# Performance work log

Measured on AMD Instinct MI355X. Metric: run time of the kernel, lower is better.

The kernel has to match this reference:

```python
import jax, jax.numpy as jnp
import numpy as np

B, P, D = 8, 576, 1024
H = 16
HD = D // H  # 64
HID = 4 * D  # 4096
EPS = 1e-6  # flax LayerNorm default


def _ln(x, g, b):
    m = jnp.mean(x, axis=-1, keepdims=True)
    v = jnp.var(x, axis=-1, keepdims=True)
    return (x - m) * jax.lax.rsqrt(v + EPS) * g + b


def setup_inputs() -> dict:
    key = jax.random.key(0)
    ks = jax.random.split(key, 8)
    s = 0.02
    return {
        "x": jax.random.normal(ks[0], (B, P, D), dtype=jnp.float32),
        "w_qkv": jax.random.normal(ks[1], (D, 3 * D), dtype=jnp.float32) * s,
        "q_g": jnp.ones((HD,), jnp.float32), "q_b": jnp.zeros((HD,), jnp.float32),
        "k_g": jnp.ones((HD,), jnp.float32), "k_b": jnp.zeros((HD,), jnp.float32),
        "o_g": jnp.ones((D,), jnp.float32), "o_b": jnp.zeros((D,), jnp.float32),
        "w_proj": jax.random.normal(ks[2], (D, D), dtype=jnp.float32) * s,
        "b_proj": jnp.zeros((D,), jnp.float32),
        "ln1_g": jnp.ones((D,), jnp.float32), "ln1_b": jnp.zeros((D,), jnp.float32),
        "ln2_g": jnp.ones((D,), jnp.float32), "ln2_b": jnp.zeros((D,), jnp.float32),
        "w1": jax.random.normal(ks[3], (D, HID), dtype=jnp.float32) * s,
        "b1": jnp.zeros((HID,), jnp.float32),
        "w2": jax.random.normal(ks[4], (HID, D), dtype=jnp.float32) * s,
        "b2": jnp.zeros((D,), jnp.float32),
        "ls1": jnp.full((D,), 1e-5, jnp.float32),
        "ls2": jnp.full((D,), 1e-5, jnp.float32),
    }


def reference(x, w_qkv, q_g, q_b, k_g, k_b, o_g, o_b, w_proj, b_proj,
              ln1_g, ln1_b, ln2_g, ln2_b, w1, b1, w2, b2, ls1, ls2):
    scale = HD ** (-0.5)
    # --- attention branch ---
    o = _ln(x, ln1_g, ln1_b)
    qkv = jnp.einsum('bpd,de->bpe', o, w_qkv)
    qkv = qkv.reshape(B, P, 3, H, HD).transpose(2, 0, 3, 1, 4)  # [3,B,H,P,HD]
    q, k, v = qkv[0], qkv[1], qkv[2]
    q = _ln(q, q_g, q_b) * scale  # QK-LayerNorm per head
    k = _ln(k, k_g, k_b)
    attn = jax.nn.softmax(jnp.einsum('bhqd,bhkd->bhqk', q, k), axis=-1)
    o = jnp.einsum('bhqk,bhkd->bhqd', attn, v)
    o = jnp.swapaxes(o, 1, 2).reshape(B, P, D)
    o = _ln(o, o_g, o_b)
    o = jnp.einsum('bpd,de->bpe', o, w_proj) + b_proj
    x = x + o * ls1
    # --- MLP branch ---
    o = _ln(x, ln2_g, ln2_b)
    o = jax.nn.gelu(jnp.einsum('bpd,dh->bph', o, w1) + b1)  # tanh-approx gelu (flax default)
    o = jnp.einsum('bph,hd->bpd', o, w2) + b2
    return x + o * ls2
```

## Files before the change

### kernel.cpp

```cpp
#include <hip/hip_runtime.h>
#include <hip/hip_bf16.h>

#define DEV static __device__ __forceinline__

typedef short frag8 __attribute__((ext_vector_type(8)));
typedef float accf4 __attribute__((ext_vector_type(4)));


DEV unsigned short f2bf(float f){
  union { float f; unsigned int u; } v; v.f = f;
  unsigned int r = v.u + 0x7fffu + ((v.u >> 16) & 1u);
  return (unsigned short)(r >> 16);
}

DEV void gload16(const void* g, void* l){
  __builtin_amdgcn_global_load_lds((const __attribute__((address_space(1))) void*)g,
                                   (__attribute__((address_space(3))) void*)l, 16, 0, 0);
}

DEV float gelu_tanh(float x){
  float u = 0.7978845608028654f * (x + 0.044715f * x * x * x);
  float e = __expf(2.0f * u);
  float th = 1.0f - 2.0f / (e + 1.0f);
  return 0.5f * x * (1.0f + th);
}

DEV void block_map(int bid, int nwg, int gx, int& tx, int& ty){
  const int swz = ((nwg & 7) == 0) ? ((bid & 7) * (nwg >> 3) + (bid >> 3)) : bid;
  const int gy = nwg / gx;
  const int cg = swz / (gy * 16);
  const int rr = swz - cg * gy * 16;
  const int gw = min(16, gx - cg * 16);
  tx = cg * 16 + rr % gw;
  ty = rr / gw;
}

__global__ __launch_bounds__(256) void wtrans(const float* __restrict__ W,
                                              unsigned short* __restrict__ Wt,
                                              int K, int N){
  __shared__ float t[32][33];
  const int n0 = blockIdx.x * 32, k0 = blockIdx.y * 32;
  const int tx = threadIdx.x, ty = threadIdx.y;
  #pragma unroll
  for (int i = 0; i < 4; i++)
    t[ty + i*8][tx] = W[(long)(k0 + ty + i*8) * N + n0 + tx];
  __syncthreads();
  #pragma unroll
  for (int i = 0; i < 4; i++)
    Wt[(long)(n0 + ty + i*8) * K + k0 + tx] = f2bf(t[tx][ty + i*8]);
}

__global__ __launch_bounds__(256) void ln_rows(const float* __restrict__ in,
                                               const float* __restrict__ g,
                                               const float* __restrict__ beta,
                                               unsigned short* __restrict__ out){
  const long row = blockIdx.x;
  const int t = threadIdx.x;
  const float4 v = ((const float4*)(in + row * 1024))[t];
  float s  = v.x + v.y + v.z + v.w;
  float s2 = v.x*v.x + v.y*v.y + v.z*v.z + v.w*v.w;
  #pragma unroll
  for (int o = 32; o; o >>= 1){ s += __shfl_xor(s, o); s2 += __shfl_xor(s2, o); }
  __shared__ float rs[4], rq[4];
  const int wv = t >> 6;
  if ((t & 63) == 0){ rs[wv] = s; rq[wv] = s2; }
  __syncthreads();
  s  = rs[0] + rs[1] + rs[2] + rs[3];
  s2 = rq[0] + rq[1] + rq[2] + rq[3];
  const float mean = s * (1.f/1024.f);
  const float inv = rsqrtf(s2 * (1.f/1024.f) - mean*mean + 1e-6f);
  const float4 gv = ((const float4*)g)[t];
  const float4 bv = ((const float4*)beta)[t];
  ushort4 o4;
  o4.x = f2bf((v.x - mean)*inv*gv.x + bv.x);
  o4.y = f2bf((v.y - mean)*inv*gv.y + bv.y);
  o4.z = f2bf((v.z - mean)*inv*gv.z + bv.z);
  o4.w = f2bf((v.w - mean)*inv*gv.w + bv.w);
  *(ushort4*)(out + row * 1024 + t * 4) = o4;
}

__global__ __launch_bounds__(256) void v_trans(const float* __restrict__ qkvVf,
                                               unsigned short* __restrict__ Vt){
  const int bh = blockIdx.x, pt = blockIdx.y;
  const int b = bh >> 4, h = bh & 15;
  __shared__ float tile[64][65];
  const int t = threadIdx.x;
  #pragma unroll
  for (int i = 0; i < 16; i++){
    int idx = i * 256 + t; int p = idx >> 6, d = idx & 63;
    tile[p][d] = qkvVf[((long)(b * 576) + pt * 64 + p) * 1024 + h * 64 + d];
  }
  __syncthreads();
  #pragma unroll
  for (int i = 0; i < 16; i++){
    int idx = i * 256 + t; int d = idx >> 6, p = idx & 63;
    Vt[((long)bh * 64 + d) * 576 + pt * 64 + p] = f2bf(tile[p][d]);
  }
}

__global__ __launch_bounds__(256) void attn_k(const unsigned short* __restrict__ Qn,
                                              const unsigned short* __restrict__ Kn,
                                              const unsigned short* __restrict__ Vt,
                                              float* __restrict__ O){
  const int qb = blockIdx.x;
  const int bh = blockIdx.y;
  const int b = bh >> 4, h = bh & 15;
  const int tid = threadIdx.x, wv = tid >> 6, lane = tid & 63;
  const int fr = lane & 15, fq = lane >> 4;
  __shared__ float S[16][578];
  __shared__ __align__(16) unsigned short Pl[16][584];

  const unsigned short* qbase = Qn + ((long)bh * 576 + qb * 16 + fr) * 64;
  frag8 qf0 = *(const frag8*)(qbase + fq * 8);
  frag8 qf1 = *(const frag8*)(qbase + 32 + fq * 8);

  for (int i = 0; i < 9; i++){
    const int kt = wv + 4 * i;
    const unsigned short* kbase = Kn + ((long)bh * 576 + kt * 16 + fr) * 64;
    frag8 kf0 = *(const frag8*)(kbase + fq * 8);
    frag8 kf1 = *(const frag8*)(kbase + 32 + fq * 8);
    accf4 a = {0.f, 0.f, 0.f, 0.f};
    a = __builtin_amdgcn_mfma_f32_16x16x32_bf16(qf0, kf0, a, 0, 0, 0);
    a = __builtin_amdgcn_mfma_f32_16x16x32_bf16(qf1, kf1, a, 0, 0, 0);
    #pragma unroll
    for (int rr = 0; rr < 4; rr++) S[fq * 4 + rr][kt * 16 + fr] = a[rr];
  }
  __syncthreads();

  {
    const int row = tid >> 4, cid = tid & 15;
    float vals[36];
    float mx = -1e30f;
    #pragma unroll
    for (int i = 0; i < 36; i++){ vals[i] = S[row][cid + 16 * i]; mx = fmaxf(mx, vals[i]); }
    #pragma unroll
    for (int o = 8; o; o >>= 1) mx = fmaxf(mx, __shfl_xor(mx, o));
    float sum = 0.f;
    #pragma unroll
    for (int i = 0; i < 36; i++){ vals[i] = __expf(vals[i] - mx); sum += vals[i]; }
    #pragma unroll
    for (int o = 8; o; o >>= 1) sum += __shfl_xor(sum, o);
    const float rsum = 1.f / sum;
    #pragma unroll
    for (int i = 0; i < 36; i++) Pl[row][cid + 16 * i] = f2bf(vals[i] * rsum);
  }
  __syncthreads();

  accf4 oa = {0.f, 0.f, 0.f, 0.f};
  for (int kt = 0; kt < 18; kt++){
    frag8 pf = *(const frag8*)&Pl[fr][kt * 32 + fq * 8];
    const unsigned short* vb = Vt + ((long)bh * 64 + wv * 16 + fr) * 576 + kt * 32 + fq * 8;
    frag8 vf = *(const frag8*)vb;
    oa = __builtin_amdgcn_mfma_f32_16x16x32_bf16(pf, vf, oa, 0, 0, 0);
  }
  #pragma unroll
  for (int rr = 0; rr < 4; rr++){
    const long orow = (long)b * 576 + qb * 16 + fq * 4 + rr;
    O[orow * 1024 + h * 64 + wv * 16 + fr] = oa[rr];
  }
}

template<int BN, int EPI>
__global__ __launch_bounds__(256) void gemm_bk64(
    const unsigned short* __restrict__ A, const unsigned short* __restrict__ Bt,
    float* __restrict__ Cf, unsigned short* __restrict__ Cb,
    const float* __restrict__ bias, const float* __restrict__ ls,
    const float* __restrict__ resid,
    const float* __restrict__ qg, const float* __restrict__ qb2,
    const float* __restrict__ kg, const float* __restrict__ kb2,
    unsigned short* __restrict__ Qn, unsigned short* __restrict__ Kn,
    float* __restrict__ Vf,
    int M, int N, int K, int gx)
{
  constexpr int NF = BN / 32;
  constexpr int BSLOT = BN / 32;
  __shared__ __align__(16) unsigned short As[2][128 * 64];
  __shared__ __align__(16) unsigned short Bs[2][BN * 64];
  const int tid = threadIdx.x;
  const int wave = tid >> 6, l = tid & 63;
  const int fr = l & 15, fq = l >> 4;
  const int wr = wave >> 1, wc = wave & 1;
  const int rsw = fr & 7;
  int tx, ty;
  block_map(blockIdx.x, gridDim.x, gx, tx, ty);
  const long rowbase = (long)ty * 128;
  const long colbase = (long)tx * BN;

  const int r8 = l >> 3;
  const int kq = (l & 7) ^ r8;
  const unsigned short* aS = A + (rowbase + wave*32 + r8) * (long)K + kq * 8;
  const unsigned short* bS = Bt + (colbase + wave*(BN/4) + r8) * (long)K + kq * 8;

  accf4 acc[4][NF];
  const accf4 zero = {0.f, 0.f, 0.f, 0.f};
  #pragma unroll
  for (int m = 0; m < 4; m++)
    #pragma unroll
    for (int n = 0; n < NF; n++) acc[m][n] = zero;

  auto stage = [&](int d, int t){
    const long k0 = (long)t * 64;
    #pragma unroll
    for (int s = 0; s < 4; s++)
      gload16(aS + (long)s * 8 * K + k0, &As[d][(wave*4 + s) * 512]);
    #pragma unroll
    for (int s = 0; s < BSLOT; s++)
      gload16(bS + (long)s * 8 * K + k0, &Bs[d][(wave*BSLOT + s) * 512]);
  };
  auto compute = [&](int d){
    #pragma unroll
    for (int kk = 0; kk < 2; kk++){
      const int csw = ((kk * 4 + fq) ^ rsw) * 8;
      frag8 bf[NF];
      #pragma unroll
      for (int n = 0; n < NF; n++)
        bf[n] = *(const frag8*)&Bs[d][(wc*(BN/2) + n*16 + fr) * 64 + csw];
      #pragma unroll
      for (int m = 0; m < 4; m++){
        frag8 af = *(const frag8*)&As[d][(wr*64 + m*16 + fr) * 64 + csw];
        #pragma unroll
        for (int n = 0; n < NF; n++)
          acc[m][n] = __builtin_amdgcn_mfma_f32_16x16x32_bf16(af, bf[n], acc[m][n], 0, 0, 0);
      }
    }
  };

  const int NT = K >> 6;
  stage(0, 0);
  __syncthreads();
  int cur = 0;
  for (int t = 0; t < NT; ++t){
    if (t + 1 < NT) stage(cur ^ 1, t + 1);
    compute(cur);
    __syncthreads();
    cur ^= 1;
  }

  if constexpr (EPI == 3){
    const int cg = (int)colbase + wc * 64;
    const int kind = cg >> 10;
    const int h = (cg & 1023) >> 6;
    if (kind < 2){
      const float* g  = kind ? kg : qg;
      const float* bb = kind ? kb2 : qb2;
      const float sc = kind ? 1.0f : 0.125f;
      unsigned short* Out = kind ? Kn : Qn;
      #pragma unroll
      for (int m = 0; m < 4; m++){
        #pragma unroll
        for (int r = 0; r < 4; r++){
          float s1 = 0.f, s2 = 0.f;
          #pragma unroll
          for (int n = 0; n < NF; n++){ const float v = acc[m][n][r]; s1 += v; s2 += v*v; }
          #pragma unroll
          for (int o = 8; o; o >>= 1){ s1 += __shfl_xor(s1, o); s2 += __shfl_xor(s2, o); }
          const float mean = s1 * (1.f/64.f);
          const float inv = rsqrtf(s2 * (1.f/64.f) - mean*mean + 1e-6f);
          const long row = rowbase + wr*64 + m*16 + fq*4 + r;
          const int bq = (int)(row / 576), p = (int)(row - (long)bq*576);
          unsigned short* dst = Out + (((long)(bq*16 + h))*576 + p)*64;
          #pragma unroll
          for (int n = 0; n < NF; n++){
            const int d = n*16 + fr;
            dst[d] = f2bf(((acc[m][n][r] - mean)*inv*g[d] + bb[d]) * sc);
          }
        }
      }
    } else {
      #pragma unroll
      for (int m = 0; m < 4; m++){
        const long rb = rowbase + wr*64 + m*16 + fq*4;
        #pragma unroll
        for (int n = 0; n < NF; n++){
          const int vc = (cg - 2048) + n*16 + fr;
          #pragma unroll
          for (int r = 0; r < 4; r++)
            Vf[(rb + r)*1024 + vc] = acc[m][n][r];
        }
      }
    }
  } else {
    #pragma unroll
    for (int m = 0; m < 4; m++){
      const long rb = rowbase + wr * 64 + m * 16 + fq * 4;
      #pragma unroll
      for (int n = 0; n < NF; n++){
        const long cb = colbase + wc * (BN/2) + n * 16 + fr;
        #pragma unroll
        for (int r = 0; r < 4; r++){
          const long idx = (rb + r) * N + cb;
          const float v = acc[m][n][r];
          if constexpr (EPI == 1){
            Cf[idx] = resid[idx] + (v + bias[cb]) * ls[cb];
          } else {
            Cb[idx] = f2bf(gelu_tanh(v + bias[cb]));
          }
        }
      }
    }
  }
}

extern "C" void kernel_launch(void* const* d_in, const int* in_sizes, int n_in,
                              void* d_out, int out_size, void* d_ws, size_t ws_size,
                              hipStream_t stream){
  (void)in_sizes; (void)n_in; (void)out_size; (void)ws_size;
  const float* x      = (const float*)d_in[0];
  const float* w_qkv  = (const float*)d_in[1];
  const float* q_g    = (const float*)d_in[2];
  const float* q_b    = (const float*)d_in[3];
  const float* k_g    = (const float*)d_in[4];
  const float* k_b    = (const float*)d_in[5];
  const float* o_g    = (const float*)d_in[6];
  const float* o_b    = (const float*)d_in[7];
  const float* w_proj = (const float*)d_in[8];
  const float* b_proj = (const float*)d_in[9];
  const float* ln1_g  = (const float*)d_in[10];
  const float* ln1_b  = (const float*)d_in[11];
  const float* ln2_g  = (const float*)d_in[12];
  const float* ln2_b  = (const float*)d_in[13];
  const float* w1     = (const float*)d_in[14];
  const float* b1     = (const float*)d_in[15];
  const float* w2     = (const float*)d_in[16];
  const float* b2     = (const float*)d_in[17];
  const float* ls1    = (const float*)d_in[18];
  const float* ls2    = (const float*)d_in[19];
  float* out = (float*)d_out;

  char* ws = (char*)d_ws;
  size_t off = 0;
  auto alloc = [&](size_t bytes)->void*{
    void* p = ws + off; off += (bytes + 255) & ~(size_t)255; return p;
  };
  unsigned short* wqkvT  = (unsigned short*)alloc(3072l*1024*2);
  unsigned short* wprojT = (unsigned short*)alloc(1024l*1024*2);
  unsigned short* w1T    = (unsigned short*)alloc(4096l*1024*2);
  unsigned short* w2T    = (unsigned short*)alloc(1024l*4096*2);
  unsigned short* xnA    = (unsigned short*)alloc(4608l*1024*2);
  float*          qkvVf  = (float*)alloc(4608l*1024*4);
  unsigned short* Qn     = (unsigned short*)alloc(73728l*64*2);
  unsigned short* Kn     = (unsigned short*)alloc(73728l*64*2);
  unsigned short* Vt     = (unsigned short*)alloc(73728l*64*2);
  unsigned short* hbf    = (unsigned short*)alloc(4608l*4096*2);
  float*          attnO  = qkvVf;

  wtrans<<<dim3(3072/32, 1024/32), dim3(32,8), 0, stream>>>(w_qkv,  wqkvT,  1024, 3072);
  wtrans<<<dim3(1024/32, 1024/32), dim3(32,8), 0, stream>>>(w_proj, wprojT, 1024, 1024);
  wtrans<<<dim3(4096/32, 1024/32), dim3(32,8), 0, stream>>>(w1,     w1T,    1024, 4096);
  wtrans<<<dim3(1024/32, 4096/32), dim3(32,8), 0, stream>>>(w2,     w2T,    4096, 1024);

  ln_rows<<<4608, 256, 0, stream>>>(x, ln1_g, ln1_b, xnA);
  gemm_bk64<128,3><<<24*36, 256, 0, stream>>>(xnA, wqkvT, nullptr, nullptr,
                                              nullptr, nullptr, nullptr,
                                              q_g, q_b, k_g, k_b, Qn, Kn, qkvVf,
                                              4608, 3072, 1024, 24);
  v_trans<<<dim3(128,9), 256, 0, stream>>>(qkvVf, Vt);
  attn_k<<<dim3(36,128), 256, 0, stream>>>(Qn, Kn, Vt, attnO);
  ln_rows<<<4608, 256, 0, stream>>>(attnO, o_g, o_b, xnA);
  gemm_bk64<64,1><<<16*36, 256, 0, stream>>>(xnA, wprojT, out, nullptr,
                                             b_proj, ls1, x,
                                             nullptr, nullptr, nullptr, nullptr,
                                             nullptr, nullptr, nullptr,
                                             4608, 1024, 1024, 16);
  ln_rows<<<4608, 256, 0, stream>>>(out, ln2_g, ln2_b, xnA);
  gemm_bk64<64,2><<<64*36, 256, 0, stream>>>(xnA, w1T, nullptr, hbf,
                                             b1, nullptr, nullptr,
                                             nullptr, nullptr, nullptr, nullptr,
                                             nullptr, nullptr, nullptr,
                                             4608, 4096, 1024, 64);
  gemm_bk64<64,1><<<16*36, 256, 0, stream>>>(hbf, w2T, out, nullptr,
                                             b2, ls2, out,
                                             nullptr, nullptr, nullptr, nullptr,
                                             nullptr, nullptr, nullptr,
                                             4608, 1024, 4096, 16);
}
```

Baseline: 305.0 us.

## Remap attention blocks per XCD, prefetch K/V fragments, alias P into S

The attention launch becomes a 1D grid whose block index is decoded so that all query blocks of a given (batch, head) land on the same XCD, which should improve L2 reuse of K and V. K and V fragment loads are software-pipelined one iteration ahead of the MFMAs. The bf16 probability buffer now aliases the fp32 score buffer to cut LDS use and allow more blocks per CU. This aliasing needs an extra barrier after the score reads, before P is written.

```diff
diff --git a/kernel.cpp b/kernel.cpp
--- a/kernel.cpp
+++ b/kernel.cpp
@@ -102,28 +102,37 @@
                                               const unsigned short* __restrict__ Kn,
                                               const unsigned short* __restrict__ Vt,
                                               float* __restrict__ O){
-  const int qb = blockIdx.x;
-  const int bh = blockIdx.y;
+  const int f = blockIdx.x;
+  const int xcd = f & 7, j = f >> 3;
+  const int bh = xcd * 16 + j / 36;
+  const int qb = j - (j / 36) * 36;
   const int b = bh >> 4, h = bh & 15;
   const int tid = threadIdx.x, wv = tid >> 6, lane = tid & 63;
   const int fr = lane & 15, fq = lane >> 4;
-  __shared__ float S[16][578];
-  __shared__ __align__(16) unsigned short Pl[16][584];
+  __shared__ __align__(16) float S[16][578];
+  unsigned short* Pl = (unsigned short*)&S[0][0];
 
   const unsigned short* qbase = Qn + ((long)bh * 576 + qb * 16 + fr) * 64;
   frag8 qf0 = *(const frag8*)(qbase + fq * 8);
   frag8 qf1 = *(const frag8*)(qbase + 32 + fq * 8);
 
+  const unsigned short* kb = Kn + ((long)bh * 576 + wv * 16 + fr) * 64 + fq * 8;
+  frag8 kf0 = *(const frag8*)(kb);
+  frag8 kf1 = *(const frag8*)(kb + 32);
   for (int i = 0; i < 9; i++){
     const int kt = wv + 4 * i;
-    const unsigned short* kbase = Kn + ((long)bh * 576 + kt * 16 + fr) * 64;
-    frag8 kf0 = *(const frag8*)(kbase + fq * 8);
-    frag8 kf1 = *(const frag8*)(kbase + 32 + fq * 8);
+    frag8 nk0 = kf0, nk1 = kf1;
+    if (i < 8){
+      const unsigned short* kbn = kb + (long)4096 * (i + 1);
+      nk0 = *(const frag8*)(kbn);
+      nk1 = *(const frag8*)(kbn + 32);
+    }
     accf4 a = {0.f, 0.f, 0.f, 0.f};
     a = __builtin_amdgcn_mfma_f32_16x16x32_bf16(qf0, kf0, a, 0, 0, 0);
     a = __builtin_amdgcn_mfma_f32_16x16x32_bf16(qf1, kf1, a, 0, 0, 0);
     #pragma unroll
     for (int rr = 0; rr < 4; rr++) S[fq * 4 + rr][kt * 16 + fr] = a[rr];
+    kf0 = nk0; kf1 = nk1;
   }
   __syncthreads();
 
@@ -133,6 +142,7 @@
     float mx = -1e30f;
     #pragma unroll
     for (int i = 0; i < 36; i++){ vals[i] = S[row][cid + 16 * i]; mx = fmaxf(mx, vals[i]); }
+    __syncthreads();
     #pragma unroll
     for (int o = 8; o; o >>= 1) mx = fmaxf(mx, __shfl_xor(mx, o));
     float sum = 0.f;
@@ -142,16 +152,19 @@
     for (int o = 8; o; o >>= 1) sum += __shfl_xor(sum, o);
     const float rsum = 1.f / sum;
     #pragma unroll
-    for (int i = 0; i < 36; i++) Pl[row][cid + 16 * i] = f2bf(vals[i] * rsum);
-  }
-  __syncthreads();
-
+    for (int i = 0; i < 36; i++) Pl[row * 584 + cid + 16 * i] = f2bf(vals[i] * rsum);
+  }
+  __syncthreads();
+
+  const unsigned short* vb = Vt + ((long)bh * 64 + wv * 16 + fr) * 576 + fq * 8;
+  frag8 vf = *(const frag8*)(vb);
   accf4 oa = {0.f, 0.f, 0.f, 0.f};
   for (int kt = 0; kt < 18; kt++){
-    frag8 pf = *(const frag8*)&Pl[fr][kt * 32 + fq * 8];
-    const unsigned short* vb = Vt + ((long)bh * 64 + wv * 16 + fr) * 576 + kt * 32 + fq * 8;
-    frag8 vf = *(const frag8*)vb;
+    frag8 nv = vf;
+    if (kt < 17) nv = *(const frag8*)(vb + (kt + 1) * 32);
+    frag8 pf = *(const frag8*)(Pl + fr * 584 + kt * 32 + fq * 8);
     oa = __builtin_amdgcn_mfma_f32_16x16x32_bf16(pf, vf, oa, 0, 0, 0);
+    vf = nv;
   }
   #pragma unroll
   for (int rr = 0; rr < 4; rr++){
@@ -355,7 +368,7 @@
                                               q_g, q_b, k_g, k_b, Qn, Kn, qkvVf,
                                               4608, 3072, 1024, 24);
   v_trans<<<dim3(128,9), 256, 0, stream>>>(qkvVf, Vt);
-  attn_k<<<dim3(36,128), 256, 0, stream>>>(Qn, Kn, Vt, attnO);
+  attn_k<<<4608, 256, 0, stream>>>(Qn, Kn, Vt, attnO);
   ln_rows<<<4608, 256, 0, stream>>>(attnO, o_g, o_b, xnA);
   gemm_bk64<64,1><<<16*36, 256, 0, stream>>>(xnA, wprojT, out, nullptr,
                                              b_proj, ls1, x,
```

New measurement: 306.5 us. About the same (+0.5%).

## Rewrite attention as flash-style online softmax with LDS-staged double-buffered K/V tiles

Applied to the files above, without the earlier changes.

The attention kernel now processes 64 queries per block (16 per wave) and streams K and V in 64-key tiles. The tiles are staged into swizzled LDS through async global_load_lds with double buffering, and an online softmax (running max and sum) replaces the full score matrix in shared memory. The block index is also remapped so all query blocks of one head land on the same XCD, which should improve L2 reuse of K and V. This cuts redundant global K/V reads across query blocks and removes the large score buffer, at the cost of per-tile rescaling work and bf16 P round-trips through LDS.

```diff
diff --git a/kernel.cpp b/kernel.cpp
--- a/kernel.cpp
+++ b/kernel.cpp
@@ -102,61 +102,107 @@
                                               const unsigned short* __restrict__ Kn,
                                               const unsigned short* __restrict__ Vt,
                                               float* __restrict__ O){
-  const int qb = blockIdx.x;
-  const int bh = blockIdx.y;
+  __shared__ __align__(16) unsigned short Ks[2][4096];
+  __shared__ __align__(16) unsigned short Vs[2][4096];
+  __shared__ __align__(16) unsigned short Plds[4096];
+  const int f = blockIdx.x;
+  const int xcd = f & 7, j = f >> 3;
+  const int bh = xcd * 16 + j / 9;
+  const int qb = j - (j / 9) * 9;
   const int b = bh >> 4, h = bh & 15;
-  const int tid = threadIdx.x, wv = tid >> 6, lane = tid & 63;
-  const int fr = lane & 15, fq = lane >> 4;
-  __shared__ float S[16][578];
-  __shared__ __align__(16) unsigned short Pl[16][584];
-
-  const unsigned short* qbase = Qn + ((long)bh * 576 + qb * 16 + fr) * 64;
-  frag8 qf0 = *(const frag8*)(qbase + fq * 8);
-  frag8 qf1 = *(const frag8*)(qbase + 32 + fq * 8);
-
-  for (int i = 0; i < 9; i++){
-    const int kt = wv + 4 * i;
-    const unsigned short* kbase = Kn + ((long)bh * 576 + kt * 16 + fr) * 64;
-    frag8 kf0 = *(const frag8*)(kbase + fq * 8);
-    frag8 kf1 = *(const frag8*)(kbase + 32 + fq * 8);
-    accf4 a = {0.f, 0.f, 0.f, 0.f};
-    a = __builtin_amdgcn_mfma_f32_16x16x32_bf16(qf0, kf0, a, 0, 0, 0);
-    a = __builtin_amdgcn_mfma_f32_16x16x32_bf16(qf1, kf1, a, 0, 0, 0);
-    #pragma unroll
-    for (int rr = 0; rr < 4; rr++) S[fq * 4 + rr][kt * 16 + fr] = a[rr];
-  }
+  const int tid = threadIdx.x, w = tid >> 6, l = tid & 63;
+  const int fr = l & 15, fq = l >> 4;
+  const int rsw = fr & 7;
+  const int q0 = qb * 64;
+
+  const unsigned short* qbase = Qn + ((long)bh * 576 + q0 + w * 16 + fr) * 64;
+  const frag8 qf0 = *(const frag8*)(qbase + fq * 8);
+  const frag8 qf1 = *(const frag8*)(qbase + 32 + fq * 8);
+
+  const int r8 = l >> 3;
+  const int kq8 = ((l & 7) ^ r8) * 8;
+  const unsigned short* kSrc = Kn + ((long)bh * 576 + w * 16 + r8) * 64 + kq8;
+  const unsigned short* vSrc = Vt + ((long)bh * 64 + w * 16 + r8) * 576 + kq8;
+
+  auto stage = [&](int d, int t){
+    gload16(kSrc + (long)t * 4096,              &Ks[d][w * 1024]);
+    gload16(kSrc + (long)t * 4096 + 512,        &Ks[d][w * 1024 + 512]);
+    gload16(vSrc + (long)t * 64,                &Vs[d][w * 1024]);
+    gload16(vSrc + (long)t * 64 + 8l * 576,     &Vs[d][w * 1024 + 512]);
+  };
+
+  accf4 oacc[4];
+  #pragma unroll
+  for (int nd = 0; nd < 4; nd++) oacc[nd] = (accf4){0.f, 0.f, 0.f, 0.f};
+  float m[4] = {-1e30f, -1e30f, -1e30f, -1e30f};
+  float lsum[4] = {0.f, 0.f, 0.f, 0.f};
+
+  stage(0, 0);
   __syncthreads();
-
-  {
-    const int row = tid >> 4, cid = tid & 15;
-    float vals[36];
-    float mx = -1e30f;
-    #pragma unroll
-    for (int i = 0; i < 36; i++){ vals[i] = S[row][cid + 16 * i]; mx = fmaxf(mx, vals[i]); }
-    #pragma unroll
-    for (int o = 8; o; o >>= 1) mx = fmaxf(mx, __shfl_xor(mx, o));
-    float sum = 0.f;
-    #pragma unroll
-    for (int i = 0; i < 36; i++){ vals[i] = __expf(vals[i] - mx); sum += vals[i]; }
-    #pragma unroll
-    for (int o = 8; o; o >>= 1) sum += __shfl_xor(sum, o);
-    const float rsum = 1.f / sum;
-    #pragma unroll
-    for (int i = 0; i < 36; i++) Pl[row][cid + 16 * i] = f2bf(vals[i] * rsum);
-  }
-  __syncthreads();
-
-  accf4 oa = {0.f, 0.f, 0.f, 0.f};
-  for (int kt = 0; kt < 18; kt++){
-    frag8 pf = *(const frag8*)&Pl[fr][kt * 32 + fq * 8];
-    const unsigned short* vb = Vt + ((long)bh * 64 + wv * 16 + fr) * 576 + kt * 32 + fq * 8;
-    frag8 vf = *(const frag8*)vb;
-    oa = __builtin_amdgcn_mfma_f32_16x16x32_bf16(pf, vf, oa, 0, 0, 0);
-  }
+  int cur = 0;
+  for (int t = 0; t < 9; ++t){
+    if (t < 8) stage(cur ^ 1, t + 1);
+
+    accf4 st[4];
+    #pragma unroll
+    for (int kt4 = 0; kt4 < 4; kt4++){
+      const int c0 = ((0 * 4 + fq) ^ rsw) * 8;
+      const int c1 = ((1 * 4 + fq) ^ rsw) * 8;
+      frag8 kf0 = *(const frag8*)&Ks[cur][(kt4 * 16 + fr) * 64 + c0];
+      frag8 kf1 = *(const frag8*)&Ks[cur][(kt4 * 16 + fr) * 64 + c1];
+      accf4 a = {0.f, 0.f, 0.f, 0.f};
+      a = __builtin_amdgcn_mfma_f32_16x16x32_bf16(qf0, kf0, a, 0, 0, 0);
+      a = __builtin_amdgcn_mfma_f32_16x16x32_bf16(qf1, kf1, a, 0, 0, 0);
+      st[kt4] = a;
+    }
+
+    #pragma unroll
+    for (int rr = 0; rr < 4; rr++){
+      float v = fmaxf(fmaxf(st[0][rr], st[1][rr]), fmaxf(st[2][rr], st[3][rr]));
+      #pragma unroll
+      for (int o = 8; o; o >>= 1) v = fmaxf(v, __shfl_xor(v, o));
+      const float mn = fmaxf(m[rr], v);
+      const float sc = __expf(m[rr] - mn);
+      float p[4], rs = 0.f;
+      #pragma unroll
+      for (int kt4 = 0; kt4 < 4; kt4++){ p[kt4] = __expf(st[kt4][rr] - mn); rs += p[kt4]; }
+      #pragma unroll
+      for (int o = 8; o; o >>= 1) rs += __shfl_xor(rs, o);
+      lsum[rr] = lsum[rr] * sc + rs;
+      m[rr] = mn;
+      #pragma unroll
+      for (int nd = 0; nd < 4; nd++) oacc[nd][rr] *= sc;
+      const int prow = fq * 4 + rr;
+      #pragma unroll
+      for (int kt4 = 0; kt4 < 4; kt4++){
+        const int chunk = kt4 * 2 + (fr >> 3);
+        Plds[w * 1024 + prow * 64 + ((chunk ^ (prow & 7)) << 3) + (fr & 7)] = f2bf(p[kt4]);
+      }
+    }
+
+    #pragma unroll
+    for (int nd = 0; nd < 4; nd++){
+      const int c0 = ((0 * 4 + fq) ^ rsw) * 8;
+      const int c1 = ((1 * 4 + fq) ^ rsw) * 8;
+      frag8 af0 = *(const frag8*)&Plds[w * 1024 + fr * 64 + c0];
+      frag8 af1 = *(const frag8*)&Plds[w * 1024 + fr * 64 + c1];
+      frag8 vf0 = *(const frag8*)&Vs[cur][(nd * 16 + fr) * 64 + c0];
+      frag8 vf1 = *(const frag8*)&Vs[cur][(nd * 16 + fr) * 64 + c1];
+      oacc[nd] = __builtin_amdgcn_mfma_f32_16x16x32_bf16(af0, vf0, oacc[nd], 0, 0, 0);
+      oacc[nd] = __builtin_amdgcn_mfma_f32_16x16x32_bf16(af1, vf1, oacc[nd], 0, 0, 0);
+    }
+
+    __syncthreads();
+    cur ^= 1;
+  }
+
   #pragma unroll
   for (int rr = 0; rr < 4; rr++){
-    const long orow = (long)b * 576 + qb * 16 + fq * 4 + rr;
-    O[orow * 1024 + h * 64 + wv * 16 + fr] = oa[rr];
+    const float rinv = 1.f / lsum[rr];
+    const long orow = (long)b * 576 + q0 + w * 16 + fq * 4 + rr;
+    #pragma unroll
+    for (int nd = 0; nd < 4; nd++)
+      O[orow * 1024 + h * 64 + nd * 16 + fr] = oacc[nd][rr] * rinv;
   }
 }
 
@@ -355,7 +401,7 @@
                                               q_g, q_b, k_g, k_b, Qn, Kn, qkvVf,
                                               4608, 3072, 1024, 24);
   v_trans<<<dim3(128,9), 256, 0, stream>>>(qkvVf, Vt);
-  attn_k<<<dim3(36,128), 256, 0, stream>>>(Qn, Kn, Vt, attnO);
+  attn_k<<<1152, 256, 0, stream>>>(Qn, Kn, Vt, attnO);
   ln_rows<<<4608, 256, 0, stream>>>(attnO, o_g, o_b, xnA);
   gemm_bk64<64,1><<<16*36, 256, 0, stream>>>(xnA, wprojT, out, nullptr,
                                              b_proj, ls1, x,
```

Measured after the change: 272.5 us. 1.12x faster.
